# Kernel tuning notes

Measured on AMD Instinct MI355X. Metric: run time of the kernel, lower is better.

## Reference

```python
import jax, jax.numpy as jnp
from jax import lax
import numpy as np

B = 8192   # samples
L = 32     # predicted chars per sample (num_chars[i])
M = 32     # target labels per sample (num_labels[i])
C = 96     # character classes


def _edit_trace(pred, tgt):
    """Levenshtein DP + backtrace for one sample.
    pred: [L] int, tgt: [M] int.
    Returns (ti, tj, valid) of length L+M: 1-based (i,j) positions of the
    diagonal (match/substitute) moves on the optimal edit path, as emitted by
    distance_and_trace; valid masks non-diagonal / out-of-path steps."""
    Ls, Ms = pred.shape[0], tgt.shape[0]
    cost = (pred[:, None] != tgt[None, :]).astype(jnp.int32)  # [L,M]
    row0 = jnp.arange(Ms + 1, dtype=jnp.int32)

    def row_step(prev, crow):
        first = prev[0] + 1
        def col_step(left, z):
            up, diag, c = z
            v = jnp.minimum(jnp.minimum(up + 1, left + 1), diag + c)
            return v, v
        _, rest = lax.scan(col_step, first, (prev[1:], prev[:-1], crow))
        new = jnp.concatenate([first[None], rest])
        return new, new

    _, rows = lax.scan(row_step, row0, cost)
    D = jnp.concatenate([row0[None, :], rows], axis=0)  # [L+1, M+1]

    def bt_step(carry, _):
        i, j = carry
        c = cost[jnp.maximum(i - 1, 0), jnp.maximum(j - 1, 0)]
        dij = D[i, j]
        diag = (i > 0) & (j > 0) & (D[i - 1, j - 1] + c == dij)
        up = (~diag) & (i > 0) & (D[i - 1, j] + 1 == dij)
        left = (~diag) & (~up) & (j > 0)
        ni = i - (diag | up).astype(jnp.int32)
        nj = j - (diag | left).astype(jnp.int32)
        return (ni, nj), (i, j, diag)

    (_, _), (ti, tj, valid) = lax.scan(
        bt_step, (jnp.int32(Ls), jnp.int32(Ms)), None, length=Ls + Ms)
    return ti, tj, valid


def _forward(x, y, num_chars, num_labels):
    b = num_chars.shape[0]
    c = x.shape[1]
    l = x.shape[0] // b
    m = y.shape[0] // b
    logits = x.reshape(b, l, c)          # [B,L,C]
    labels = y.reshape(b, m)             # [B,M]
    pred = jnp.argmax(logits, axis=-1)   # torch.max(x,1) indices
    ti, tj, valid = jax.vmap(_edit_trace)(pred, labels)  # [B, L+M] each
    logp = jax.nn.log_softmax(logits, axis=-1)
    xi = jnp.where(valid, ti - 1, 0)     # trace[:,0]-1 (+ per-sample offset via reshape)
    yi = jnp.where(valid, tj - 1, 0)     # trace[:,1]-1
    lab = jnp.take_along_axis(labels, yi, axis=1)                 # [B,L+M]
    lp = jnp.take_along_axis(logp, xi[..., None], axis=1)         # [B,L+M,C]
    ce = -jnp.take_along_axis(lp, lab[..., None], axis=2)[..., 0]  # [B,L+M]
    cnt = valid.sum(axis=1)
    per_sample = jnp.where(valid, ce, 0.0).sum(axis=1) / jnp.maximum(cnt, 1)
    nonempty = cnt > 0                   # attenuation: skip empty traces
    total = jnp.where(nonempty, per_sample, 0.0).sum()
    return total / nonempty.sum()


def setup_inputs() -> dict:
    key = jax.random.key(0)
    k1, k2 = jax.random.split(key)
    x = jax.random.normal(k1, (B * L, C), dtype=jnp.float32)
    y = jax.random.randint(k2, (B * M,), 0, C, dtype=jnp.int32)
    num_chars = jnp.full((B,), L, dtype=jnp.int32)
    num_labels = jnp.full((B,), M, dtype=jnp.int32)
    return {"x": x, "y": y, "num_chars": num_chars, "num_labels": num_labels}


def reference(x, y, num_chars, num_labels):
    return _forward(x, y, num_chars, num_labels)
```

## Files before the change

### kernel.cpp

```cpp
#include <hip/hip_runtime.h>
#include <stdint.h>

#define BNUM  8192
#define LROWS 32
#define MLAB  32
#define CCLS  96
#define WPB   4
#define SPW   2
#define SPB   (WPB*SPW)
#define NBLK  (BNUM/SPB)

typedef float f32x4 __attribute__((ext_vector_type(4)));

__device__ __forceinline__ int dpp_wshr1_i32(int v) {
    return __builtin_amdgcn_update_dpp(0, v, 0x138, 0xF, 0xF, true);
}
__device__ __forceinline__ float dpp_wshr1_f32(float v) {
    return __int_as_float(
        __builtin_amdgcn_update_dpp(0, __float_as_int(v), 0x138, 0xF, 0xF, true));
}

__global__ __launch_bounds__(256, 3) void editloss_main(
    const float* __restrict__ x, const int* __restrict__ y,
    float* __restrict__ partial_sum, float* __restrict__ partial_cnt)
{
    __shared__ float  ceTab[SPB][LROWS * MLAB];
    __shared__ float2 lpS[SPB][LROWS];
    __shared__ float  psum[SPB];
    __shared__ float  pcnt[SPB];

    const int w    = threadIdx.x >> 6;
    const int lane = threadIdx.x & 63;
    const int g    = lane >> 5;
    const int u    = lane & 31;
    const int s    = w * SPW + g;
    const int sb   = blockIdx.x * SPB + s;

    const float* xs    = x + (size_t)sb * (LROWS * CCLS);
    const int    lab_u = y[sb * MLAB + u];

    const f32x4* rowv = (const f32x4*)(xs + (size_t)u * CCLS);
    f32x4 va[24];
#pragma unroll
    for (int t = 0; t < 24; ++t) va[t] = rowv[t];

    const float* gcol = xs + lab_u;
    float xg[LROWS];
#pragma unroll
    for (int r = 0; r < LROWS; ++r) xg[r] = gcol[r * CCLS];

    asm volatile("" :
        "+v"(va[0]),  "+v"(va[1]),  "+v"(va[2]),  "+v"(va[3]),
        "+v"(va[4]),  "+v"(va[5]),  "+v"(va[6]),  "+v"(va[7]),
        "+v"(va[8]),  "+v"(va[9]),  "+v"(va[10]), "+v"(va[11]),
        "+v"(va[12]), "+v"(va[13]), "+v"(va[14]), "+v"(va[15]),
        "+v"(va[16]), "+v"(va[17]), "+v"(va[18]), "+v"(va[19]),
        "+v"(va[20]), "+v"(va[21]), "+v"(va[22]), "+v"(va[23]));
    asm volatile("" :
        "+v"(xg[0]),  "+v"(xg[1]),  "+v"(xg[2]),  "+v"(xg[3]),
        "+v"(xg[4]),  "+v"(xg[5]),  "+v"(xg[6]),  "+v"(xg[7]),
        "+v"(xg[8]),  "+v"(xg[9]),  "+v"(xg[10]), "+v"(xg[11]),
        "+v"(xg[12]), "+v"(xg[13]), "+v"(xg[14]), "+v"(xg[15]),
        "+v"(xg[16]), "+v"(xg[17]), "+v"(xg[18]), "+v"(xg[19]),
        "+v"(xg[20]), "+v"(xg[21]), "+v"(xg[22]), "+v"(xg[23]),
        "+v"(xg[24]), "+v"(xg[25]), "+v"(xg[26]), "+v"(xg[27]),
        "+v"(xg[28]), "+v"(xg[29]), "+v"(xg[30]), "+v"(xg[31])
        :: "memory");

    {
        float bmax[4]; int bidx[4]; float bsum[4];
#pragma unroll
        for (int c = 0; c < 4; ++c) { bmax[c] = -1e30f; bidx[c] = 0; bsum[c] = 0.f; }
#pragma unroll
        for (int t = 0; t < 24; ++t) {
            const int c = t / 6;
            const f32x4 v = va[t];
            const int base = t * 4;
            if (v[0] > bmax[c]) { bmax[c] = v[0]; bidx[c] = base + 0; }
            if (v[1] > bmax[c]) { bmax[c] = v[1]; bidx[c] = base + 1; }
            if (v[2] > bmax[c]) { bmax[c] = v[2]; bidx[c] = base + 2; }
            if (v[3] > bmax[c]) { bmax[c] = v[3]; bidx[c] = base + 3; }
            bsum[c] += __expf(v[0]) + __expf(v[1]) + __expf(v[2]) + __expf(v[3]);
        }
        float m = bmax[0]; int idx = bidx[0];
#pragma unroll
        for (int c = 1; c < 4; ++c)
            if (bmax[c] > m) { m = bmax[c]; idx = bidx[c]; }
        const float lse = __logf((bsum[0] + bsum[1]) + (bsum[2] + bsum[3]));
        lpS[s][u] = make_float2(lse, (float)idx);
    }
    asm volatile("s_waitcnt lgkmcnt(0)" ::: "memory");

    {
        const float fl = (float)lab_u;
#pragma unroll
        for (int r = 0; r < LROWS; ++r) {
            const float2 lp = lpS[s][r];
            const float  ce = lp.x - xg[r];
            ceTab[s][r * MLAB + u] = (lp.y == fl) ? ce : -ce;
        }
    }
    asm volatile("s_waitcnt lgkmcnt(0)" ::: "memory");

    const int j = u + 1;
    int   prevW = 0;   float prevCE = 0.f;
    int   diagW = 0;   float diagCE = 0.f;
#pragma unroll 4
    for (int d = 1; d <= LROWS + MLAB; ++d) {
        const int   lWs  = dpp_wshr1_i32(prevW);
        const float lCEs = dpp_wshr1_f32(prevCE);
        const int i = d - j;
        const int   lW  = (u == 0) ? max(i, 0)     : lWs;
        const float lCE = (u == 0) ? 0.f           : lCEs;
        const int   dW  = (u == 0) ? max(i - 1, 0) : diagW;
        const float dCE = (u == 0) ? 0.f           : diagCE;
        int curW; float curCE;
        if (i <= 0) {
            curW = j; curCE = 0.f;
        } else if (i > LROWS) {
            curW = prevW; curCE = prevCE;
        } else {
            const int uD = prevW & 255, uC = prevW >> 8;
            const int lD = lW & 255,    lC = lW >> 8;
            const int dD = dW & 255,    dC = dW >> 8;
            const float ct  = ceTab[s][(i - 1) * MLAB + u];
            const int   c   = (ct < 0.f) ? 1 : 0;
            const int nD = min(min(uD, lD) + 1, dD + c);
            const bool dg = (dD + c == nD);
            const bool up = !dg && (uD + 1 == nD);
            int nC; float nCE;
            if (dg)      { nC = dC + 1; nCE = dCE + fabsf(ct); }
            else if (up) { nC = uC;     nCE = prevCE;          }
            else         { nC = lC;     nCE = lCE;             }
            curW = nD | (nC << 8);
            curCE = nCE;
        }
        diagW = lWs; diagCE = lCEs;
        prevW = curW; prevCE = curCE;
    }

    if (u == 31) {
        const int cnt = prevW >> 8;
        psum[s] = (cnt > 0) ? prevCE / (float)cnt : 0.f;
        pcnt[s] = (cnt > 0) ? 1.f : 0.f;
    }
    __syncthreads();
    if (threadIdx.x == 0) {
        float ss = 0.f, cc = 0.f;
#pragma unroll
        for (int k = 0; k < SPB; ++k) { ss += psum[k]; cc += pcnt[k]; }
        partial_sum[blockIdx.x] = ss;
        partial_cnt[blockIdx.x] = cc;
    }
}

__global__ __launch_bounds__(256) void editloss_finalize(
    const float* __restrict__ partial_sum, const float* __restrict__ partial_cnt,
    float* __restrict__ out, int nblocks)
{
    float s = 0.f, c = 0.f;
    for (int k = threadIdx.x; k < nblocks; k += 256) {
        s += partial_sum[k];
        c += partial_cnt[k];
    }
#pragma unroll
    for (int d = 32; d >= 1; d >>= 1) {
        s += __shfl_xor(s, d);
        c += __shfl_xor(c, d);
    }
    __shared__ float ss[4], cc[4];
    const int w = threadIdx.x >> 6, lane = threadIdx.x & 63;
    if (lane == 0) { ss[w] = s; cc[w] = c; }
    __syncthreads();
    if (threadIdx.x == 0) {
        const float S  = ss[0] + ss[1] + ss[2] + ss[3];
        const float C2 = cc[0] + cc[1] + cc[2] + cc[3];
        out[0] = (C2 > 0.f) ? (S / C2) : 0.f;
    }
}

extern "C" void kernel_launch(void* const* d_in, const int* in_sizes, int n_in,
                              void* d_out, int out_size, void* d_ws, size_t ws_size,
                              hipStream_t stream) {
    const float* x = (const float*)d_in[0];
    const int*   y = (const int*)d_in[1];
    float* out = (float*)d_out;

    float* partial_sum = (float*)d_ws;
    float* partial_cnt = partial_sum + NBLK;

    editloss_main<<<NBLK, 256, 0, stream>>>(x, y, partial_sum, partial_cnt);
    editloss_finalize<<<1, 256, 0, stream>>>(partial_sum, partial_cnt, out, NBLK);
}
```

Before: 163.9 us.

## Split fused kernel into CE-table producer and DP consumer kernels

Splits the single kernel into two. The first computes argmax, log-sum-exp and the signed cross-entropy table and writes it to a global workspace. The second loads that table into shared memory and runs the anti-diagonal edit-distance DP. The aim is to lower register and LDS pressure in each kernel so more waves fit per CU. The cost is a global round trip of about 32 MB of CE table plus an extra kernel launch.

```diff
diff --git a/kernel.cpp b/kernel.cpp
--- a/kernel.cpp
+++ b/kernel.cpp
@@ -9,6 +9,7 @@
 #define SPW   2
 #define SPB   (WPB*SPW)
 #define NBLK  (BNUM/SPB)
+#define CEF   (LROWS*MLAB)
 
 typedef float f32x4 __attribute__((ext_vector_type(4)));
 
@@ -20,14 +21,11 @@
         __builtin_amdgcn_update_dpp(0, __float_as_int(v), 0x138, 0xF, 0xF, true));
 }
 
-__global__ __launch_bounds__(256, 3) void editloss_main(
+__global__ __launch_bounds__(256, 3) void editloss_k1(
     const float* __restrict__ x, const int* __restrict__ y,
-    float* __restrict__ partial_sum, float* __restrict__ partial_cnt)
+    float* __restrict__ ceG)
 {
-    __shared__ float  ceTab[SPB][LROWS * MLAB];
     __shared__ float2 lpS[SPB][LROWS];
-    __shared__ float  psum[SPB];
-    __shared__ float  pcnt[SPB];
 
     const int w    = threadIdx.x >> 6;
     const int lane = threadIdx.x & 63;
@@ -93,14 +91,38 @@
 
     {
         const float fl = (float)lab_u;
+        float* ceRow = ceG + (size_t)sb * CEF;
 #pragma unroll
         for (int r = 0; r < LROWS; ++r) {
             const float2 lp = lpS[s][r];
             const float  ce = lp.x - xg[r];
-            ceTab[s][r * MLAB + u] = (lp.y == fl) ? ce : -ce;
+            ceRow[r * MLAB + u] = (lp.y == fl) ? ce : -ce;
         }
     }
-    asm volatile("s_waitcnt lgkmcnt(0)" ::: "memory");
+}
+
+__global__ __launch_bounds__(256, 4) void editloss_k2(
+    const float* __restrict__ ceG,
+    float* __restrict__ partial_sum, float* __restrict__ partial_cnt)
+{
+    __shared__ float  ceTab[SPB][CEF];
+    __shared__ float  psum[SPB];
+    __shared__ float  pcnt[SPB];
+
+    const int w    = threadIdx.x >> 6;
+    const int lane = threadIdx.x & 63;
+    const int g    = lane >> 5;
+    const int u    = lane & 31;
+    const int s    = w * SPW + g;
+
+    {
+        const f32x4* src = (const f32x4*)(ceG + (size_t)blockIdx.x * (SPB * CEF));
+        f32x4* dst = (f32x4*)&ceTab[0][0];
+#pragma unroll
+        for (int t = 0; t < 8; ++t)
+            dst[t * 256 + threadIdx.x] = src[t * 256 + threadIdx.x];
+    }
+    __syncthreads();
 
     const int j = u + 1;
     int   prevW = 0;   float prevCE = 0.f;
@@ -186,9 +208,11 @@
     const int*   y = (const int*)d_in[1];
     float* out = (float*)d_out;
 
-    float* partial_sum = (float*)d_ws;
+    float* ceG         = (float*)d_ws;
+    float* partial_sum = ceG + (size_t)BNUM * CEF;
     float* partial_cnt = partial_sum + NBLK;
 
-    editloss_main<<<NBLK, 256, 0, stream>>>(x, y, partial_sum, partial_cnt);
+    editloss_k1<<<NBLK, 256, 0, stream>>>(x, y, ceG);
+    editloss_k2<<<NBLK, 256, 0, stream>>>(ceG, partial_sum, partial_cnt);
     editloss_finalize<<<1, 256, 0, stream>>>(partial_sum, partial_cnt, out, NBLK);
 }
```

Result: slower. 178.9 us (+9.2%).

## Assign DP rows to lanes and build cost table locally without LDS round trip

Applied to the files above, without the earlier changes.

The wavefront DP now maps each lane to a prediction row instead of a target column, so every lane already holds its own log-sum-exp and argmax. The lpS shared staging and one LDS wait are removed, and each lane gathers the logits at all 32 labels of its own row, in rotated order, to fill its row of the cost table. The per-lane target loads and scattered global gathers rise (32 label reads plus 32 indexed logit reads per lane). The LDS store pattern also changes: rotation avoids bank conflicts, but the DP reads ceTab[u*32+jcol-1], a stride-32 access that may conflict.

```diff
diff --git a/kernel.cpp b/kernel.cpp
--- a/kernel.cpp
+++ b/kernel.cpp
@@ -24,10 +24,9 @@
     const float* __restrict__ x, const int* __restrict__ y,
     float* __restrict__ partial_sum, float* __restrict__ partial_cnt)
 {
-    __shared__ float  ceTab[SPB][LROWS * MLAB];
-    __shared__ float2 lpS[SPB][LROWS];
-    __shared__ float  psum[SPB];
-    __shared__ float  pcnt[SPB];
+    __shared__ float ceTab[SPB][LROWS * MLAB];
+    __shared__ float psum[SPB];
+    __shared__ float pcnt[SPB];
 
     const int w    = threadIdx.x >> 6;
     const int lane = threadIdx.x & 63;
@@ -36,18 +35,22 @@
     const int s    = w * SPW + g;
     const int sb   = blockIdx.x * SPB + s;
 
-    const float* xs    = x + (size_t)sb * (LROWS * CCLS);
-    const int    lab_u = y[sb * MLAB + u];
+    const float* xs   = x + (size_t)sb * (LROWS * CCLS);
+    const float* rowp = xs + (size_t)u * CCLS;
+    const int*   yrow = y + sb * MLAB;
 
-    const f32x4* rowv = (const f32x4*)(xs + (size_t)u * CCLS);
+    const f32x4* rowv = (const f32x4*)rowp;
     f32x4 va[24];
 #pragma unroll
     for (int t = 0; t < 24; ++t) va[t] = rowv[t];
 
-    const float* gcol = xs + lab_u;
-    float xg[LROWS];
+    float xr[32];
 #pragma unroll
-    for (int r = 0; r < LROWS; ++r) xg[r] = gcol[r * CCLS];
+    for (int k = 0; k < 32; ++k) {
+        const int c    = (k + u) & 31;
+        const int labc = yrow[c];
+        xr[k] = rowp[labc];
+    }
 
     asm volatile("" :
         "+v"(va[0]),  "+v"(va[1]),  "+v"(va[2]),  "+v"(va[3]),
@@ -57,16 +60,17 @@
         "+v"(va[16]), "+v"(va[17]), "+v"(va[18]), "+v"(va[19]),
         "+v"(va[20]), "+v"(va[21]), "+v"(va[22]), "+v"(va[23]));
     asm volatile("" :
-        "+v"(xg[0]),  "+v"(xg[1]),  "+v"(xg[2]),  "+v"(xg[3]),
-        "+v"(xg[4]),  "+v"(xg[5]),  "+v"(xg[6]),  "+v"(xg[7]),
-        "+v"(xg[8]),  "+v"(xg[9]),  "+v"(xg[10]), "+v"(xg[11]),
-        "+v"(xg[12]), "+v"(xg[13]), "+v"(xg[14]), "+v"(xg[15]),
-        "+v"(xg[16]), "+v"(xg[17]), "+v"(xg[18]), "+v"(xg[19]),
-        "+v"(xg[20]), "+v"(xg[21]), "+v"(xg[22]), "+v"(xg[23]),
-        "+v"(xg[24]), "+v"(xg[25]), "+v"(xg[26]), "+v"(xg[27]),
-        "+v"(xg[28]), "+v"(xg[29]), "+v"(xg[30]), "+v"(xg[31])
+        "+v"(xr[0]),  "+v"(xr[1]),  "+v"(xr[2]),  "+v"(xr[3]),
+        "+v"(xr[4]),  "+v"(xr[5]),  "+v"(xr[6]),  "+v"(xr[7]),
+        "+v"(xr[8]),  "+v"(xr[9]),  "+v"(xr[10]), "+v"(xr[11]),
+        "+v"(xr[12]), "+v"(xr[13]), "+v"(xr[14]), "+v"(xr[15]),
+        "+v"(xr[16]), "+v"(xr[17]), "+v"(xr[18]), "+v"(xr[19]),
+        "+v"(xr[20]), "+v"(xr[21]), "+v"(xr[22]), "+v"(xr[23]),
+        "+v"(xr[24]), "+v"(xr[25]), "+v"(xr[26]), "+v"(xr[27]),
+        "+v"(xr[28]), "+v"(xr[29]), "+v"(xr[30]), "+v"(xr[31])
         :: "memory");
 
+    float lse; int idx;
     {
         float bmax[4]; int bidx[4]; float bsum[4];
 #pragma unroll
@@ -82,60 +86,56 @@
             if (v[3] > bmax[c]) { bmax[c] = v[3]; bidx[c] = base + 3; }
             bsum[c] += __expf(v[0]) + __expf(v[1]) + __expf(v[2]) + __expf(v[3]);
         }
-        float m = bmax[0]; int idx = bidx[0];
+        float m = bmax[0]; idx = bidx[0];
 #pragma unroll
         for (int c = 1; c < 4; ++c)
             if (bmax[c] > m) { m = bmax[c]; idx = bidx[c]; }
-        const float lse = __logf((bsum[0] + bsum[1]) + (bsum[2] + bsum[3]));
-        lpS[s][u] = make_float2(lse, (float)idx);
+        lse = __logf((bsum[0] + bsum[1]) + (bsum[2] + bsum[3]));
+    }
+
+#pragma unroll
+    for (int k = 0; k < 32; ++k) {
+        const int   c    = (k + u) & 31;
+        const int   labc = yrow[c];
+        const float cv   = lse - xr[k];
+        ceTab[s][u * MLAB + c] = (idx == labc) ? cv : -cv;
     }
     asm volatile("s_waitcnt lgkmcnt(0)" ::: "memory");
 
-    {
-        const float fl = (float)lab_u;
-#pragma unroll
-        for (int r = 0; r < LROWS; ++r) {
-            const float2 lp = lpS[s][r];
-            const float  ce = lp.x - xg[r];
-            ceTab[s][r * MLAB + u] = (lp.y == fl) ? ce : -ce;
-        }
-    }
-    asm volatile("s_waitcnt lgkmcnt(0)" ::: "memory");
-
-    const int j = u + 1;
+    const int iRow = u + 1;
     int   prevW = 0;   float prevCE = 0.f;
     int   diagW = 0;   float diagCE = 0.f;
 #pragma unroll 4
     for (int d = 1; d <= LROWS + MLAB; ++d) {
-        const int   lWs  = dpp_wshr1_i32(prevW);
-        const float lCEs = dpp_wshr1_f32(prevCE);
-        const int i = d - j;
-        const int   lW  = (u == 0) ? max(i, 0)     : lWs;
-        const float lCE = (u == 0) ? 0.f           : lCEs;
-        const int   dW  = (u == 0) ? max(i - 1, 0) : diagW;
-        const float dCE = (u == 0) ? 0.f           : diagCE;
+        const int   uWs  = dpp_wshr1_i32(prevW);
+        const float uCEs = dpp_wshr1_f32(prevCE);
+        const int jcol = d - iRow;
+        const int   uW  = (u == 0) ? max(jcol, 0)     : uWs;
+        const float uCE = (u == 0) ? 0.f              : uCEs;
+        const int   dW  = (u == 0) ? max(jcol - 1, 0) : diagW;
+        const float dCE = (u == 0) ? 0.f              : diagCE;
         int curW; float curCE;
-        if (i <= 0) {
-            curW = j; curCE = 0.f;
-        } else if (i > LROWS) {
+        if (jcol <= 0) {
+            curW = iRow; curCE = 0.f;
+        } else if (jcol > MLAB) {
             curW = prevW; curCE = prevCE;
         } else {
-            const int uD = prevW & 255, uC = prevW >> 8;
-            const int lD = lW & 255,    lC = lW >> 8;
+            const int lD = prevW & 255, lC = prevW >> 8;
+            const int uD = uW & 255,    uC = uW >> 8;
             const int dD = dW & 255,    dC = dW >> 8;
-            const float ct  = ceTab[s][(i - 1) * MLAB + u];
+            const float ct  = ceTab[s][u * MLAB + (jcol - 1)];
             const int   c   = (ct < 0.f) ? 1 : 0;
             const int nD = min(min(uD, lD) + 1, dD + c);
             const bool dg = (dD + c == nD);
             const bool up = !dg && (uD + 1 == nD);
             int nC; float nCE;
             if (dg)      { nC = dC + 1; nCE = dCE + fabsf(ct); }
-            else if (up) { nC = uC;     nCE = prevCE;          }
-            else         { nC = lC;     nCE = lCE;             }
+            else if (up) { nC = uC;     nCE = uCE;             }
+            else         { nC = lC;     nCE = prevCE;          }
             curW = nD | (nC << 8);
             curCE = nCE;
         }
-        diagW = lWs; diagCE = lCEs;
+        diagW = uWs; diagCE = uCEs;
         prevW = curW; prevCE = curCE;
     }
 
```

Result: slower. 240.3 us (+46.7%).
